# Kernel tuning notes

Hardware: AMD Instinct MI355X
Metric: run time of the kernel (lower is better)

Reference implementation:

```python
import jax, jax.numpy as jnp
import numpy as np

B, S, H, NH = 8, 1024, 1024, 16
DH = H // NH


def setup_inputs() -> dict:
    key = jax.random.key(0)
    ks = jax.random.split(key, 16)
    inp = {
        'v': jax.random.normal(ks[0], (B, S, H), jnp.float32),
        'k': jax.random.normal(ks[1], (B, S, H), jnp.float32),
        'q': jax.random.normal(ks[2], (B, S, H), jnp.float32),
        'r': jax.random.normal(ks[3], (B, S, H), jnp.float32),
        'mask': jax.random.randint(ks[4], (B, 1, 1, S), 0, 2).astype(jnp.bool_),
    }
    scale = 1.0 / np.sqrt(H)
    names = ['Wv', 'Wk', 'Wq', 'Wr', 'Wm']
    for i, n in enumerate(names):
        inp[n] = jax.random.normal(ks[5 + i], (H, H), jnp.float32) * scale
        inp['b' + n[1:]] = jnp.zeros((H,), jnp.float32)
    return inp


def _heads(x, W, b):
    # torch Linear: x @ W.T + b, then split heads -> [B, NH, S, DH]
    y = jnp.einsum('bsh,oh->bso', x, W) + b
    return y.reshape(B, S, NH, DH).transpose(0, 2, 1, 3)


def reference(v, k, q, r, mask, Wv, bv, Wk, bk, Wq, bq, Wr, br, Wm, bm):
    vh = _heads(v, Wv, bv)
    kh = _heads(k, Wk, bk)
    qh = _heads(q, Wq, bq)
    rh = _heads(r, Wr, br)
    # relation-augmented scores: (QK^T + RK^T) / sqrt(d_k)
    scores = jnp.einsum('bhqd,bhkd->bhqk', qh + rh, kh) / jnp.sqrt(jnp.asarray(DH, qh.dtype))
    scores = jnp.where(mask, jnp.asarray(-1e9, scores.dtype), scores)
    att = jax.nn.softmax(scores, axis=-1)  # dropout = identity in eval
    out = jnp.einsum('bhqk,bhkd->bhqd', att, vh)
    out = out.transpose(0, 2, 1, 3).reshape(B, S, H)
    return jnp.einsum('bsh,oh->bso', out, Wm) + bm
```

## Files before the change

kernel.cpp:

```cpp
#include <hip/hip_runtime.h>
#include <hip/hip_bf16.h>
#include <stdint.h>

typedef __attribute__((ext_vector_type(4))) float f32x4;
typedef __attribute__((ext_vector_type(8))) short s16x8;
typedef __attribute__((ext_vector_type(4))) short s16x4;
typedef __attribute__((ext_vector_type(4))) int i32x4;

typedef const __attribute__((address_space(1))) unsigned glb_u32;
typedef __attribute__((address_space(3))) unsigned lds_u32;

#define DEVI __device__ __forceinline__

DEVI short f2b(float f) {
    union { float f; unsigned u; } v; v.f = f;
    unsigned r = v.u + 0x7fffu + ((v.u >> 16) & 1u);
    return (short)(r >> 16);
}

DEVI float vexp2(float x) {
    float r;
    asm("v_exp_f32 %0, %1" : "=v"(r) : "v"(x));
    return r;
}

DEVI unsigned cvtpk(float lo, float hi) {
    unsigned d;
    asm("v_cvt_pk_bf16_f32 %0, %1, %2" : "=v"(d) : "v"(lo), "v"(hi));
    return d;
}

DEVI s16x8 pack8(const f32x4& a, const f32x4& b) {
    union { unsigned u[4]; s16x8 v; } w;
    w.u[0] = cvtpk(a[0], a[1]);
    w.u[1] = cvtpk(a[2], a[3]);
    w.u[2] = cvtpk(b[0], b[1]);
    w.u[3] = cvtpk(b[2], b[3]);
    return w.v;
}

#define QSCL 0.18033688011112042f
#define MASKV -1.4426950408889634e9f

struct Ptr5 { const float* p[5]; };
struct Ptr4 { const float* p[4]; };

__global__ __launch_bounds__(256) void cvtW(Ptr5 src, short* __restrict__ dst) {
    const float* s = src.p[blockIdx.y];
    short* d = dst + (size_t)blockIdx.y * (1024u * 1024u);
    int i = (blockIdx.x * 256 + threadIdx.x) * 8;
    f32x4 a = *(const f32x4*)(s + i);
    f32x4 b = *(const f32x4*)(s + i + 4);
    s16x8 o;
#pragma unroll
    for (int j = 0; j < 4; ++j) { o[j] = f2b(a[j]); o[4 + j] = f2b(b[j]); }
    *(s16x8*)(d + i) = o;
}

__global__ __launch_bounds__(256) void cvtA(Ptr4 src, short* __restrict__ dst) {
    const float* s = src.p[blockIdx.y];
    short* d = dst + (size_t)blockIdx.y * (8u * 1024u * 1024u);
    int i = (blockIdx.x * 256 + threadIdx.x) * 8;
    f32x4 a = *(const f32x4*)(s + i);
    f32x4 b = *(const f32x4*)(s + i + 4);
    s16x8 o;
#pragma unroll
    for (int j = 0; j < 4; ++j) { o[j] = f2b(a[j]); o[4 + j] = f2b(b[j]); }
    *(s16x8*)(d + i) = o;
}

template<int AF32, int OUTMODE, int TWO>
__global__ __launch_bounds__(256) void gemm_nt(
    const void* __restrict__ A0_, const void* __restrict__ A1_,
    const short* __restrict__ W0, const short* __restrict__ W1,
    const float* __restrict__ b0, const float* __restrict__ b1,
    void* __restrict__ C_)
{
    constexpr int K = 1024, N = 1024;
    const int tid = threadIdx.x;
    const int lane = tid & 63, wid = tid >> 6;
    const int wm = wid >> 1, wn = wid & 1;
    const int r = lane & 15, g = lane >> 4;

    const int bid = blockIdx.x;
    const int logical = (bid & 7) * 64 + (bid >> 3);
    const int n0 = (logical & 7) * 128, m0 = (logical >> 3) * 128;

    __shared__ alignas(16) short As[2][128 * 32];
    __shared__ alignas(16) short Ws[2][128 * 32];

    auto stage_async = [&](int buf, int kt) {
        int kk = kt * 32;
        const short* Ap = (const short*)A0_; const short* Wp = W0;
        if (TWO && kk >= 1024) { Ap = (const short*)A1_; Wp = W1; kk &= 1023; }
#pragma unroll
        for (int i = 0; i < 2; ++i) {
            int row = wid * 32 + i * 16 + (lane >> 2);
            const short* ga = Ap + (size_t)(m0 + row) * K + kk + (lane & 3) * 8;
            const short* gw = Wp + (size_t)(n0 + row) * K + kk + (lane & 3) * 8;
            __builtin_amdgcn_global_load_lds((glb_u32*)ga,
                (lds_u32*)&As[buf][(wid * 32 + i * 16) * 32], 16, 0, 0);
            __builtin_amdgcn_global_load_lds((glb_u32*)gw,
                (lds_u32*)&Ws[buf][(wid * 32 + i * 16) * 32], 16, 0, 0);
        }
    };

    const int srow = tid >> 1, shalf = tid & 1;
    f32x4 a0g, a1g, a2g, a3g;
    s16x8 wg0, wg1;
    auto load_regs = [&](int kt) {
        int kk = kt * 32;
        const short* wp = W0 + (size_t)(n0 + srow) * K + kk + shalf * 16;
        wg0 = *(const s16x8*)wp;
        wg1 = *(const s16x8*)(wp + 8);
        const float* ap = (const float*)A0_ + (size_t)(m0 + srow) * K + kk + shalf * 16;
        a0g = *(const f32x4*)ap;       a1g = *(const f32x4*)(ap + 4);
        a2g = *(const f32x4*)(ap + 8); a3g = *(const f32x4*)(ap + 12);
    };
    auto store_lds = [&](int buf) {
        s16x8 s0, s1;
#pragma unroll
        for (int j = 0; j < 4; ++j) {
            s0[j] = f2b(a0g[j]); s0[4 + j] = f2b(a1g[j]);
            s1[j] = f2b(a2g[j]); s1[4 + j] = f2b(a3g[j]);
        }
        char* ab = (char*)As[buf];
        *(s16x8*)(ab + srow * 64 + shalf * 32) = s0;
        *(s16x8*)(ab + srow * 64 + shalf * 32 + 16) = s1;
        char* wb = (char*)Ws[buf];
        *(s16x8*)(wb + srow * 64 + shalf * 32) = wg0;
        *(s16x8*)(wb + srow * 64 + shalf * 32 + 16) = wg1;
    };

    f32x4 z = {0.f, 0.f, 0.f, 0.f};
    f32x4 acc[4][4];
#pragma unroll
    for (int i = 0; i < 4; ++i)
#pragma unroll
        for (int j = 0; j < 4; ++j) acc[i][j] = z;

    auto compute = [&](int buf) {
        s16x8 af[4], bfr[4];
#pragma unroll
        for (int f = 0; f < 4; ++f) {
            af[f]  = *(const s16x8*)&As[buf][(wm * 64 + f * 16 + r) * 32 + g * 8];
            bfr[f] = *(const s16x8*)&Ws[buf][(wn * 64 + f * 16 + r) * 32 + g * 8];
        }
#pragma unroll
        for (int i = 0; i < 4; ++i)
#pragma unroll
            for (int j = 0; j < 4; ++j)
                acc[i][j] = __builtin_amdgcn_mfma_f32_16x16x32_bf16(af[i], bfr[j], acc[i][j], 0, 0, 0);
    };

    constexpr int NK = TWO ? 64 : 32;
    if constexpr (AF32) { load_regs(0); store_lds(0); }
    else stage_async(0, 0);
    __syncthreads();
    int buf = 0;
    for (int kt = 0; kt < NK; ++kt) {
        if (kt + 1 < NK) {
            if constexpr (AF32) load_regs(kt + 1);
            else stage_async(buf ^ 1, kt + 1);
        }
        compute(buf);
        if (AF32 && kt + 1 < NK) store_lds(buf ^ 1);
        __syncthreads();
        buf ^= 1;
    }

#pragma unroll
    for (int j = 0; j < 4; ++j) {
        int col = n0 + wn * 64 + j * 16 + r;
        float bb = b0[col];
        if (TWO) bb += b1[col];
#pragma unroll
        for (int i = 0; i < 4; ++i) {
            int rowb = m0 + wm * 64 + i * 16 + g * 4;
            if constexpr (OUTMODE == 2) {
                int bb_ = rowb >> 10, tok = rowb & 1023;
                int tokp = (tok & ~31) | (((tok >> 2) & 3) << 3) | (((tok >> 4) & 1) << 2);
                short* dst = (short*)C_ + ((size_t)(bb_ * 16 + (col >> 6))) * 65536
                           + (size_t)(col & 63) * 1024 + tokp;
                s16x4 o;
#pragma unroll
                for (int q = 0; q < 4; ++q) o[q] = f2b(acc[i][j][q] + bb);
                *(s16x4*)dst = o;
            } else {
#pragma unroll
                for (int q = 0; q < 4; ++q) {
                    float val = acc[i][j][q] + bb;
                    if constexpr (OUTMODE == 1)
                        ((float*)C_)[(size_t)(rowb + q) * N + col] = val;
                    else if constexpr (OUTMODE == 3)
                        ((short*)C_)[(size_t)(rowb + q) * N + col] = f2b(val * QSCL);
                    else
                        ((short*)C_)[(size_t)(rowb + q) * N + col] = f2b(val);
                }
            }
        }
    }
}

__global__ __launch_bounds__(256) void attn_fwd(
    const short* __restrict__ qrh, const short* __restrict__ kh,
    const short* __restrict__ vT, const int* __restrict__ mask,
    short* __restrict__ outp)
{
    const int bh = blockIdx.x;
    const int b = bh >> 4, h = bh & 15;
    const int qt = blockIdx.y;
    const int tid = threadIdx.x, lane = tid & 63, wid = tid >> 6;
    const int r = lane & 15, g = lane >> 4;

    __shared__ alignas(16) short Ks[64 * 64];
    __shared__ alignas(16) short Vs[64 * 64];
    __shared__ alignas(16) float mb[1024];

    {
        i32x4 mi = *(const i32x4*)(mask + b * 1024 + tid * 4);
        f32x4 mv;
#pragma unroll
        for (int j = 0; j < 4; ++j) mv[j] = mi[j] ? MASKV : 0.f;
        *(f32x4*)&mb[tid * 4] = mv;
    }

    const int q0 = qt * 128 + wid * 32;
    const short* qbA = qrh + (size_t)(b * 1024 + q0 + r) * 1024 + h * 64;
    const short* qbB = qbA + 16 * 1024;
    s16x8 qA0 = *(const s16x8*)(qbA + g * 8);
    s16x8 qA1 = *(const s16x8*)(qbA + 32 + g * 8);
    s16x8 qB0 = *(const s16x8*)(qbB + g * 8);
    s16x8 qB1 = *(const s16x8*)(qbB + 32 + g * 8);

    f32x4 z = {0.f, 0.f, 0.f, 0.f};
    f32x4 oA[4], oB[4];
#pragma unroll
    for (int i = 0; i < 4; ++i) { oA[i] = z; oB[i] = z; }
    float lA = 0.f, lB = 0.f;

    const int srow = tid >> 2, sq = tid & 3;
    const short* kg = kh + (size_t)(b * 1024 + srow) * 1024 + h * 64 + sq * 16;
    const short* vg = vT + ((size_t)(b * 16 + h)) * 65536 + (size_t)srow * 1024 + sq * 16;
    const int p0s = (sq * 2) ^ (srow & 7), p1s = (sq * 2 + 1) ^ (srow & 7);

    s16x8 kr0, kr1, vr0, vr1;
    auto stage_load = [&](int t) {
        const short* kp = kg + (size_t)(t * 64) * 1024;
        kr0 = *(const s16x8*)kp; kr1 = *(const s16x8*)(kp + 8);
        const short* vp = vg + t * 64;
        vr0 = *(const s16x8*)vp; vr1 = *(const s16x8*)(vp + 8);
    };
    auto stage_write = [&]() {
        char* kb2 = (char*)Ks;
        *(s16x8*)(kb2 + srow * 128 + p0s * 16) = kr0;
        *(s16x8*)(kb2 + srow * 128 + p1s * 16) = kr1;
        char* vb2 = (char*)Vs;
        *(s16x8*)(vb2 + srow * 128 + p0s * 16) = vr0;
        *(s16x8*)(vb2 + srow * 128 + p1s * 16) = vr1;
    };

    stage_load(0);
    for (int t = 0; t < 16; ++t) {
        if (t) __syncthreads();
        stage_write();
        __syncthreads();
        if (t < 15) stage_load(t + 1);

        f32x4 pA[4], pB[4];
        char* kb2 = (char*)Ks;
        float tsA = 0.f, tsB = 0.f;
#pragma unroll
        for (int fn = 0; fn < 4; ++fn) {
            int row = fn * 16 + r;
            s16x8 kfa = *(const s16x8*)(kb2 + row * 128 + ((g ^ (row & 7)) << 4));
            s16x8 kfb = *(const s16x8*)(kb2 + row * 128 + (((4 + g) ^ (row & 7)) << 4));
            f32x4 cA = __builtin_amdgcn_mfma_f32_16x16x32_bf16(kfa, qA0, z, 0, 0, 0);
            cA = __builtin_amdgcn_mfma_f32_16x16x32_bf16(kfb, qA1, cA, 0, 0, 0);
            f32x4 cB = __builtin_amdgcn_mfma_f32_16x16x32_bf16(kfa, qB0, z, 0, 0, 0);
            cB = __builtin_amdgcn_mfma_f32_16x16x32_bf16(kfb, qB1, cB, 0, 0, 0);
            f32x4 mv = *(const f32x4*)&mb[t * 64 + fn * 16 + g * 4];
#pragma unroll
            for (int qi = 0; qi < 4; ++qi) {
                float eA = vexp2(cA[qi] + mv[qi]); pA[fn][qi] = eA; tsA += eA;
                float eB = vexp2(cB[qi] + mv[qi]); pB[fn][qi] = eB; tsB += eB;
            }
        }
        tsA += __shfl_xor(tsA, 16); tsA += __shfl_xor(tsA, 32);
        tsB += __shfl_xor(tsB, 16); tsB += __shfl_xor(tsB, 32);
        lA += tsA; lB += tsB;

        char* vb2 = (char*)Vs;
#pragma unroll
        for (int ks = 0; ks < 2; ++ks) {
            s16x8 pbA = pack8(pA[2 * ks], pA[2 * ks + 1]);
            s16x8 pbB = pack8(pB[2 * ks], pB[2 * ks + 1]);
#pragma unroll
            for (int df = 0; df < 4; ++df) {
                int row = df * 16 + r;
                int slot = (ks * 4 + g) ^ (row & 7);
                s16x8 vf = *(const s16x8*)(vb2 + row * 128 + (slot << 4));
                oA[df] = __builtin_amdgcn_mfma_f32_16x16x32_bf16(vf, pbA, oA[df], 0, 0, 0);
                oB[df] = __builtin_amdgcn_mfma_f32_16x16x32_bf16(vf, pbB, oB[df], 0, 0, 0);
            }
        }
    }

    float ivA = 1.f / lA, ivB = 1.f / lB;
#pragma unroll
    for (int df = 0; df < 4; ++df) {
        s16x4 oa, ob;
#pragma unroll
        for (int qi = 0; qi < 4; ++qi) {
            oa[qi] = f2b(oA[df][qi] * ivA);
            ob[qi] = f2b(oB[df][qi] * ivB);
        }
        *(s16x4*)&outp[(size_t)(b * 1024 + q0 + r) * 1024 + h * 64 + df * 16 + g * 4] = oa;
        *(s16x4*)&outp[(size_t)(b * 1024 + q0 + 16 + r) * 1024 + h * 64 + df * 16 + g * 4] = ob;
    }
}

extern "C" void kernel_launch(void* const* d_in, const int* in_sizes, int n_in,
                              void* d_out, int out_size, void* d_ws, size_t ws_size,
                              hipStream_t stream) {
    const float* v  = (const float*)d_in[0];
    const float* k  = (const float*)d_in[1];
    const float* q  = (const float*)d_in[2];
    const float* rr = (const float*)d_in[3];
    const int* mask = (const int*)d_in[4];
    const float* Wv = (const float*)d_in[5];  const float* bv = (const float*)d_in[6];
    const float* Wk = (const float*)d_in[7];  const float* bk = (const float*)d_in[8];
    const float* Wq = (const float*)d_in[9];  const float* bq = (const float*)d_in[10];
    const float* Wr = (const float*)d_in[11]; const float* br = (const float*)d_in[12];
    const float* Wm = (const float*)d_in[13]; const float* bm = (const float*)d_in[14];

    const size_t MB = 1048576u;
    const size_t NEED_FULL = 90u * MB;
    const size_t NEED_B    = 74u * MB;
    char* ws = (char*)d_ws;
    short* Wb = (short*)ws;

    Ptr5 p5;
    p5.p[0] = Wv; p5.p[1] = Wk; p5.p[2] = Wq; p5.p[3] = Wr; p5.p[4] = Wm;
    cvtW<<<dim3(512, 5), 256, 0, stream>>>(p5, Wb);

    const short* Wvb = Wb, *Wkb = Wb + 1048576u, *Wqb = Wb + 2097152u,
               *Wrb = Wb + 3145728u, *Wmb = Wb + 4194304u;
    dim3 gg(512);

    if (ws_size >= NEED_FULL) {
        short* vb  = (short*)(ws + 10u * MB);
        short* kb  = vb + 8388608u;
        short* qb  = kb + 8388608u;
        short* rb  = qb + 8388608u;
        short* vtb = rb + 8388608u;
        short* khb = vb;
        short* qrb = kb;
        short* att = qb;

        Ptr4 p4; p4.p[0] = v; p4.p[1] = k; p4.p[2] = q; p4.p[3] = rr;
        cvtA<<<dim3(4096, 4), 256, 0, stream>>>(p4, vb);

        gemm_nt<0, 2, 0><<<gg, 256, 0, stream>>>(vb, nullptr, Wvb, nullptr, bv, nullptr, vtb);
        gemm_nt<0, 0, 0><<<gg, 256, 0, stream>>>(kb, nullptr, Wkb, nullptr, bk, nullptr, khb);
        gemm_nt<0, 3, 1><<<gg, 256, 0, stream>>>(qb, rb, Wqb, Wrb, bq, br, qrb);
        attn_fwd<<<dim3(128, 8), 256, 0, stream>>>(qrb, khb, vtb, mask, att);
        gemm_nt<0, 1, 0><<<gg, 256, 0, stream>>>(att, nullptr, Wmb, nullptr, bm, nullptr, (float*)d_out);
    } else if (ws_size >= NEED_B) {
        short* kb  = (short*)(ws + 10u * MB);
        short* qb  = kb + 8388608u;
        short* rb  = qb + 8388608u;
        short* qrb = rb + 8388608u;
        short* vtb = qb;
        short* khb = rb;
        short* att = kb;

        Ptr4 p4; p4.p[0] = k; p4.p[1] = q; p4.p[2] = rr; p4.p[3] = k;
        cvtA<<<dim3(4096, 3), 256, 0, stream>>>(p4, kb);

        gemm_nt<0, 3, 1><<<gg, 256, 0, stream>>>(qb, rb, Wqb, Wrb, bq, br, qrb);
        gemm_nt<1, 2, 0><<<gg, 256, 0, stream>>>(v, nullptr, Wvb, nullptr, bv, nullptr, vtb);
        gemm_nt<0, 0, 0><<<gg, 256, 0, stream>>>(kb, nullptr, Wkb, nullptr, bk, nullptr, khb);
        attn_fwd<<<dim3(128, 8), 256, 0, stream>>>(qrb, khb, vtb, mask, att);
        gemm_nt<0, 1, 0><<<gg, 256, 0, stream>>>(att, nullptr, Wmb, nullptr, bm, nullptr, (float*)d_out);
    }
}
```

Before: 238.3 us.

## Merge conversions and QKVR projections into single launches, fuse q/r fp32 conversion

Folds the weight and activation conversions into one cvt_all kernel, and stops converting q and r to bf16 up front. The Q+R projection now reads fp32 directly through the register-staged path. The three projection GEMMs (V, K, QR) run as one 1536-block proj_all launch via a shared gemm_body, which removes launch gaps and tail underutilization between them. The trade-off is that the QR part uses the synchronous register-load path, which may stall more than the async LDS loads. The smaller-workspace fallback is also dropped, so the function now returns without computing anything when the workspace is under 90MB.

```diff
diff --git a/kernel.cpp b/kernel.cpp
--- a/kernel.cpp
+++ b/kernel.cpp
@@ -42,52 +42,38 @@
 #define QSCL 0.18033688011112042f
 #define MASKV -1.4426950408889634e9f
 
-struct Ptr5 { const float* p[5]; };
-struct Ptr4 { const float* p[4]; };
-
-__global__ __launch_bounds__(256) void cvtW(Ptr5 src, short* __restrict__ dst) {
-    const float* s = src.p[blockIdx.y];
-    short* d = dst + (size_t)blockIdx.y * (1024u * 1024u);
-    int i = (blockIdx.x * 256 + threadIdx.x) * 8;
+struct Ptr7 { const float* p[7]; };
+
+__global__ __launch_bounds__(256) void cvt_all(Ptr7 t, short* __restrict__ vb,
+                                               short* __restrict__ kb,
+                                               short* __restrict__ Wb) {
+    int bid = blockIdx.x;
+    const float* s; short* d; int off;
+    if (bid < 4096)      { s = t.p[0]; d = vb; off = bid; }
+    else if (bid < 8192) { s = t.p[1]; d = kb; off = bid - 4096; }
+    else {
+        int w = (bid - 8192) >> 9;
+        s = t.p[2 + w]; d = Wb + (size_t)w * 1048576u; off = (bid - 8192) & 511;
+    }
+    int i = (off * 256 + threadIdx.x) * 8;
     f32x4 a = *(const f32x4*)(s + i);
     f32x4 b = *(const f32x4*)(s + i + 4);
-    s16x8 o;
-#pragma unroll
-    for (int j = 0; j < 4; ++j) { o[j] = f2b(a[j]); o[4 + j] = f2b(b[j]); }
-    *(s16x8*)(d + i) = o;
-}
-
-__global__ __launch_bounds__(256) void cvtA(Ptr4 src, short* __restrict__ dst) {
-    const float* s = src.p[blockIdx.y];
-    short* d = dst + (size_t)blockIdx.y * (8u * 1024u * 1024u);
-    int i = (blockIdx.x * 256 + threadIdx.x) * 8;
-    f32x4 a = *(const f32x4*)(s + i);
-    f32x4 b = *(const f32x4*)(s + i + 4);
-    s16x8 o;
-#pragma unroll
-    for (int j = 0; j < 4; ++j) { o[j] = f2b(a[j]); o[4 + j] = f2b(b[j]); }
-    *(s16x8*)(d + i) = o;
+    *(s16x8*)(d + i) = pack8(a, b);
 }
 
 template<int AF32, int OUTMODE, int TWO>
-__global__ __launch_bounds__(256) void gemm_nt(
-    const void* __restrict__ A0_, const void* __restrict__ A1_,
-    const short* __restrict__ W0, const short* __restrict__ W1,
-    const float* __restrict__ b0, const float* __restrict__ b1,
-    void* __restrict__ C_)
+DEVI void gemm_body(int logical,
+                    const void* A0_, const void* A1_,
+                    const short* W0, const short* W1,
+                    const float* b0, const float* b1,
+                    void* C_, short* As, short* Ws)
 {
     constexpr int K = 1024, N = 1024;
     const int tid = threadIdx.x;
     const int lane = tid & 63, wid = tid >> 6;
     const int wm = wid >> 1, wn = wid & 1;
     const int r = lane & 15, g = lane >> 4;
-
-    const int bid = blockIdx.x;
-    const int logical = (bid & 7) * 64 + (bid >> 3);
     const int n0 = (logical & 7) * 128, m0 = (logical >> 3) * 128;
-
-    __shared__ alignas(16) short As[2][128 * 32];
-    __shared__ alignas(16) short Ws[2][128 * 32];
 
     auto stage_async = [&](int buf, int kt) {
         int kk = kt * 32;
@@ -99,9 +85,9 @@
             const short* ga = Ap + (size_t)(m0 + row) * K + kk + (lane & 3) * 8;
             const short* gw = Wp + (size_t)(n0 + row) * K + kk + (lane & 3) * 8;
             __builtin_amdgcn_global_load_lds((glb_u32*)ga,
-                (lds_u32*)&As[buf][(wid * 32 + i * 16) * 32], 16, 0, 0);
+                (lds_u32*)(As + buf * 4096 + (wid * 32 + i * 16) * 32), 16, 0, 0);
             __builtin_amdgcn_global_load_lds((glb_u32*)gw,
-                (lds_u32*)&Ws[buf][(wid * 32 + i * 16) * 32], 16, 0, 0);
+                (lds_u32*)(Ws + buf * 4096 + (wid * 32 + i * 16) * 32), 16, 0, 0);
         }
     };
 
@@ -110,24 +96,22 @@
     s16x8 wg0, wg1;
     auto load_regs = [&](int kt) {
         int kk = kt * 32;
-        const short* wp = W0 + (size_t)(n0 + srow) * K + kk + shalf * 16;
+        const float* Ap = (const float*)A0_; const short* Wp = W0;
+        if (TWO && kk >= 1024) { Ap = (const float*)A1_; Wp = W1; kk &= 1023; }
+        const short* wp = Wp + (size_t)(n0 + srow) * K + kk + shalf * 16;
         wg0 = *(const s16x8*)wp;
         wg1 = *(const s16x8*)(wp + 8);
-        const float* ap = (const float*)A0_ + (size_t)(m0 + srow) * K + kk + shalf * 16;
+        const float* ap = Ap + (size_t)(m0 + srow) * K + kk + shalf * 16;
         a0g = *(const f32x4*)ap;       a1g = *(const f32x4*)(ap + 4);
         a2g = *(const f32x4*)(ap + 8); a3g = *(const f32x4*)(ap + 12);
     };
     auto store_lds = [&](int buf) {
-        s16x8 s0, s1;
-#pragma unroll
-        for (int j = 0; j < 4; ++j) {
-            s0[j] = f2b(a0g[j]); s0[4 + j] = f2b(a1g[j]);
-            s1[j] = f2b(a2g[j]); s1[4 + j] = f2b(a3g[j]);
-        }
-        char* ab = (char*)As[buf];
+        s16x8 s0 = pack8(a0g, a1g);
+        s16x8 s1 = pack8(a2g, a3g);
+        char* ab = (char*)(As + buf * 4096);
         *(s16x8*)(ab + srow * 64 + shalf * 32) = s0;
         *(s16x8*)(ab + srow * 64 + shalf * 32 + 16) = s1;
-        char* wb = (char*)Ws[buf];
+        char* wb = (char*)(Ws + buf * 4096);
         *(s16x8*)(wb + srow * 64 + shalf * 32) = wg0;
         *(s16x8*)(wb + srow * 64 + shalf * 32 + 16) = wg1;
     };
@@ -143,8 +127,8 @@
         s16x8 af[4], bfr[4];
 #pragma unroll
         for (int f = 0; f < 4; ++f) {
-            af[f]  = *(const s16x8*)&As[buf][(wm * 64 + f * 16 + r) * 32 + g * 8];
-            bfr[f] = *(const s16x8*)&Ws[buf][(wn * 64 + f * 16 + r) * 32 + g * 8];
+            af[f]  = *(const s16x8*)(As + buf * 4096 + (wm * 64 + f * 16 + r) * 32 + g * 8);
+            bfr[f] = *(const s16x8*)(Ws + buf * 4096 + (wn * 64 + f * 16 + r) * 32 + g * 8);
         }
 #pragma unroll
         for (int i = 0; i < 4; ++i)
@@ -200,6 +184,41 @@
             }
         }
     }
+}
+
+__global__ __launch_bounds__(256) void proj_all(
+    const short* __restrict__ vb, const short* __restrict__ kb,
+    const float* __restrict__ qf, const float* __restrict__ rf,
+    const short* __restrict__ Wb,
+    const float* __restrict__ bv, const float* __restrict__ bk,
+    const float* __restrict__ bq, const float* __restrict__ br,
+    short* __restrict__ vtb, short* __restrict__ khb, short* __restrict__ qrb)
+{
+    __shared__ alignas(16) short As[2 * 128 * 32];
+    __shared__ alignas(16) short Ws[2 * 128 * 32];
+    const int bid = blockIdx.x;
+    const int sub = bid >> 9, lbid = bid & 511;
+    const int logical = (lbid & 7) * 64 + (lbid >> 3);
+    if (sub == 0)
+        gemm_body<0, 2, 0>(logical, vb, nullptr, Wb, nullptr, bv, nullptr, vtb, As, Ws);
+    else if (sub == 1)
+        gemm_body<0, 0, 0>(logical, kb, nullptr, Wb + 1048576u, nullptr, bk, nullptr, khb, As, Ws);
+    else
+        gemm_body<1, 3, 1>(logical, qf, rf, Wb + 2097152u, Wb + 3145728u, bq, br, qrb, As, Ws);
+}
+
+template<int AF32, int OUTMODE, int TWO>
+__global__ __launch_bounds__(256) void gemm_nt(
+    const void* __restrict__ A0_, const void* __restrict__ A1_,
+    const short* __restrict__ W0, const short* __restrict__ W1,
+    const float* __restrict__ b0, const float* __restrict__ b1,
+    void* __restrict__ C_)
+{
+    __shared__ alignas(16) short As[2 * 128 * 32];
+    __shared__ alignas(16) short Ws[2 * 128 * 32];
+    const int bid = blockIdx.x;
+    const int logical = (bid & 7) * 64 + (bid >> 3);
+    gemm_body<AF32, OUTMODE, TWO>(logical, A0_, A1_, W0, W1, b0, b1, C_, As, Ws);
 }
 
 __global__ __launch_bounds__(256) void attn_fwd(
@@ -335,53 +354,28 @@
     const float* Wm = (const float*)d_in[13]; const float* bm = (const float*)d_in[14];
 
     const size_t MB = 1048576u;
-    const size_t NEED_FULL = 90u * MB;
-    const size_t NEED_B    = 74u * MB;
+    const size_t NEED = 90u * MB;
+    if (ws_size < NEED) return;
+
     char* ws = (char*)d_ws;
-    short* Wb = (short*)ws;
-
-    Ptr5 p5;
-    p5.p[0] = Wv; p5.p[1] = Wk; p5.p[2] = Wq; p5.p[3] = Wr; p5.p[4] = Wm;
-    cvtW<<<dim3(512, 5), 256, 0, stream>>>(p5, Wb);
-
-    const short* Wvb = Wb, *Wkb = Wb + 1048576u, *Wqb = Wb + 2097152u,
-               *Wrb = Wb + 3145728u, *Wmb = Wb + 4194304u;
-    dim3 gg(512);
-
-    if (ws_size >= NEED_FULL) {
-        short* vb  = (short*)(ws + 10u * MB);
-        short* kb  = vb + 8388608u;
-        short* qb  = kb + 8388608u;
-        short* rb  = qb + 8388608u;
-        short* vtb = rb + 8388608u;
-        short* khb = vb;
-        short* qrb = kb;
-        short* att = qb;
-
-        Ptr4 p4; p4.p[0] = v; p4.p[1] = k; p4.p[2] = q; p4.p[3] = rr;
-        cvtA<<<dim3(4096, 4), 256, 0, stream>>>(p4, vb);
-
-        gemm_nt<0, 2, 0><<<gg, 256, 0, stream>>>(vb, nullptr, Wvb, nullptr, bv, nullptr, vtb);
-        gemm_nt<0, 0, 0><<<gg, 256, 0, stream>>>(kb, nullptr, Wkb, nullptr, bk, nullptr, khb);
-        gemm_nt<0, 3, 1><<<gg, 256, 0, stream>>>(qb, rb, Wqb, Wrb, bq, br, qrb);
-        attn_fwd<<<dim3(128, 8), 256, 0, stream>>>(qrb, khb, vtb, mask, att);
-        gemm_nt<0, 1, 0><<<gg, 256, 0, stream>>>(att, nullptr, Wmb, nullptr, bm, nullptr, (float*)d_out);
-    } else if (ws_size >= NEED_B) {
-        short* kb  = (short*)(ws + 10u * MB);
-        short* qb  = kb + 8388608u;
-        short* rb  = qb + 8388608u;
-        short* qrb = rb + 8388608u;
-        short* vtb = qb;
-        short* khb = rb;
-        short* att = kb;
-
-        Ptr4 p4; p4.p[0] = k; p4.p[1] = q; p4.p[2] = rr; p4.p[3] = k;
-        cvtA<<<dim3(4096, 3), 256, 0, stream>>>(p4, kb);
-
-        gemm_nt<0, 3, 1><<<gg, 256, 0, stream>>>(qb, rb, Wqb, Wrb, bq, br, qrb);
-        gemm_nt<1, 2, 0><<<gg, 256, 0, stream>>>(v, nullptr, Wvb, nullptr, bv, nullptr, vtb);
-        gemm_nt<0, 0, 0><<<gg, 256, 0, stream>>>(kb, nullptr, Wkb, nullptr, bk, nullptr, khb);
-        attn_fwd<<<dim3(128, 8), 256, 0, stream>>>(qrb, khb, vtb, mask, att);
-        gemm_nt<0, 1, 0><<<gg, 256, 0, stream>>>(att, nullptr, Wmb, nullptr, bm, nullptr, (float*)d_out);
-    }
-}
+    short* Wb  = (short*)ws;
+    short* vb  = (short*)(ws + 10u * MB);
+    short* kb  = (short*)(ws + 26u * MB);
+    short* vtb = (short*)(ws + 42u * MB);
+    short* khb = (short*)(ws + 58u * MB);
+    short* qrb = (short*)(ws + 74u * MB);
+    short* att = vb;
+
+    Ptr7 t7;
+    t7.p[0] = v;  t7.p[1] = k;
+    t7.p[2] = Wv; t7.p[3] = Wk; t7.p[4] = Wq; t7.p[5] = Wr; t7.p[6] = Wm;
+    cvt_all<<<dim3(10752), 256, 0, stream>>>(t7, vb, kb, Wb);
+
+    proj_all<<<dim3(1536), 256, 0, stream>>>(vb, kb, q, rr, Wb,
+                                             bv, bk, bq, br, vtb, khb, qrb);
+
+    attn_fwd<<<dim3(128, 8), 256, 0, stream>>>(qrb, khb, vtb, mask, att);
+
+    gemm_nt<0, 1, 0><<<dim3(512), 256, 0, stream>>>(att, nullptr, Wb + 4194304u,
+                                                    nullptr, bm, nullptr, (float*)d_out);
+}
```

Result: faster. 223.3 us (median of 2 runs) (-6.3%).
